# Optimization experiments

Hardware: AMD Instinct MI355X
Metric: run time of the kernel (lower is better)

The kernel has to match this reference:

```python
import jax, jax.numpy as jnp
import numpy as np

ROPE_BASE = 10000.0

def _rope_cos_sin(T, d, dtype):
    inv_freq = 1.0 / (ROPE_BASE ** (jnp.arange(0, d, 2, dtype=jnp.float32) / d))
    t = jnp.arange(T, dtype=jnp.float32)
    freqs = t[:, None] * inv_freq[None, :]           # [T, d/2]
    emb = jnp.concatenate([freqs, freqs], axis=-1)   # [T, d]
    return jnp.cos(emb).astype(dtype), jnp.sin(emb).astype(dtype)

def _rotate_half(x):
    x1, x2 = jnp.split(x, 2, axis=-1)
    return jnp.concatenate([-x2, x1], axis=-1)

def setup_inputs() -> dict:
    key = jax.random.key(0)
    k1, k2, k3, k4 = jax.random.split(key, 4)
    B, T, C, H = 4, 4096, 1024, 64
    x = jax.random.normal(k1, (B, T, C), dtype=jnp.float32)
    s = 1.0 / np.sqrt(C)
    Wq = jax.random.normal(k2, (H, C), dtype=jnp.float32) * s
    Wk = jax.random.normal(k3, (H, C), dtype=jnp.float32) * s
    Wv = jax.random.normal(k4, (H, C), dtype=jnp.float32) * s
    return {"x": x, "Wq": Wq, "Wk": Wk, "Wv": Wv}

def reference(x, Wq, Wk, Wv):
    B, T, C = x.shape
    H = Wq.shape[0]
    q = jnp.einsum('btc,hc->bth', x, Wq)
    k = jnp.einsum('btc,hc->bth', x, Wk)
    v = jnp.einsum('btc,hc->bth', x, Wv)
    cos, sin = _rope_cos_sin(T, H, x.dtype)
    q = q * cos + _rotate_half(q) * sin
    k = k * cos + _rotate_half(k) * sin
    # NOTE: original scales by dim_model**-0.5 (C), not head_size
    wei = jnp.einsum('bth,bsh->bts', q, k) * (C ** -0.5)
    causal = jnp.tril(jnp.ones((T, T), dtype=bool))
    wei = jnp.where(causal, wei, -jnp.inf)
    wei = jax.nn.softmax(wei, axis=-1)
    # dropout p=0.0 (identity)
    out = jnp.einsum('bts,bsh->bth', wei, v)
    return out
```

## Files before the change

kernel.cpp:

```cpp
#include <hip/hip_runtime.h>
#include <hip/hip_bf16.h>
#include <math.h>

typedef __attribute__((ext_vector_type(8))) __bf16 bf16x8;
typedef __attribute__((ext_vector_type(4))) float f32x4;
typedef __attribute__((ext_vector_type(16))) float f32x16;
typedef __attribute__((ext_vector_type(4))) float float4_t;
typedef __attribute__((ext_vector_type(4))) unsigned int uint4_t;

#define NB 4
#define TSEQ 4096
#define CD 1024
#define HD 64
#define NCH 8
#define CHT 8
#define QBL 16

static __device__ __forceinline__ unsigned short f2bf(float f) {
    union { float f; unsigned u; } v; v.f = f;
    unsigned r = v.u + 0x7fffu + ((v.u >> 16) & 1u);
    return (unsigned short)(r >> 16);
}
static __device__ __forceinline__ float bf2f(unsigned short u) {
    union { unsigned int i; float f; } v; v.i = ((unsigned int)u) << 16;
    return v.f;
}
static __device__ __forceinline__ unsigned int pk2(float a, float b) {
    union { __bf16 h[2]; unsigned int u; } x;
    x.h[0] = (__bf16)a; x.h[1] = (__bf16)b;
    return x.u;
}

__global__ __launch_bounds__(256) void wcvt_kernel(const float* __restrict__ wq,
                                                   const float* __restrict__ wk,
                                                   const float* __restrict__ wv,
                                                   unsigned short* __restrict__ wb) {
    int i = blockIdx.x * 256 + threadIdx.x;
    int j = i >> 10;
    int col = i & 1023;
    int jb = j >> 4, off = j & 15;
    int sub = ((jb & 1) << 5) | ((jb & 2) << 3);
    int srcrow = (jb < 8) ? (sub + off) : ((jb - 8) * 16 + off);
    const float* src = (jb < 4) ? wq : ((jb < 8) ? wk : wv);
    wb[i] = f2bf(src[srcrow * 1024 + col]);
}

__global__ __launch_bounds__(256) void qkv_kernel(const float* __restrict__ x,
                                                  const unsigned short* __restrict__ wb,
                                                  unsigned short* __restrict__ qo,
                                                  unsigned short* __restrict__ ko,
                                                  unsigned short* __restrict__ vt) {
    __shared__ unsigned short xs[64][72];
    __shared__ unsigned short ws[64][72];
    const int tid = threadIdx.x;
    const int wave = tid >> 6, lane = tid & 63;
    const int lr = lane & 15;
    const int lk = (lane >> 4) << 3;
    const int rowg = (lane >> 4) << 2;
    const int row0 = blockIdx.x * 64;
    const int cbi = blockIdx.y;
    const int cb = cbi * 64;

    f32x4 acc[4];
#pragma unroll
    for (int i = 0; i < 4; ++i) acc[i] = (f32x4){0.f, 0.f, 0.f, 0.f};

    const int sr = tid >> 2;
    const int sc = (tid & 3) << 4;

    for (int k0 = 0; k0 < CD; k0 += 64) {
        __syncthreads();
        {
            const float4_t* s4 =
                reinterpret_cast<const float4_t*>(x + (size_t)(row0 + sr) * CD + k0 + sc);
            float4_t f0 = s4[0], f1 = s4[1], f2 = s4[2], f3 = s4[3];
            uint4_t w0, w1;
            w0[0] = pk2(f0[0], f0[1]); w0[1] = pk2(f0[2], f0[3]);
            w0[2] = pk2(f1[0], f1[1]); w0[3] = pk2(f1[2], f1[3]);
            w1[0] = pk2(f2[0], f2[1]); w1[1] = pk2(f2[2], f2[3]);
            w1[2] = pk2(f3[0], f3[1]); w1[3] = pk2(f3[2], f3[3]);
            *reinterpret_cast<uint4_t*>(&xs[sr][sc]) = w0;
            *reinterpret_cast<uint4_t*>(&xs[sr][sc + 8]) = w1;
        }
        {
            const uint4_t* wsrc =
                reinterpret_cast<const uint4_t*>(wb + (size_t)(cb + sr) * CD + k0 + sc);
            *reinterpret_cast<uint4_t*>(&ws[sr][sc]) = wsrc[0];
            *reinterpret_cast<uint4_t*>(&ws[sr][sc + 8]) = wsrc[1];
        }
        __syncthreads();
#pragma unroll
        for (int kk = 0; kk < 2; ++kk) {
            bf16x8 a = *reinterpret_cast<const bf16x8*>(&xs[wave * 16 + lr][kk * 32 + lk]);
#pragma unroll
            for (int c = 0; c < 4; ++c) {
                bf16x8 bfr = *reinterpret_cast<const bf16x8*>(&ws[c * 16 + lr][kk * 32 + lk]);
                acc[c] = __builtin_amdgcn_mfma_f32_16x16x32_bf16(a, bfr, acc[c], 0, 0, 0);
            }
        }
    }

    const int gr0 = row0 + wave * 16 + rowg;
    const int bidx = gr0 >> 12;
    const int tb = gr0 & (TSEQ - 1);
    if (cbi < 2) {
        unsigned short* o = (cbi == 0) ? qo : ko;
        const float sc2 = (cbi == 0) ? 0.045084218764560315f : 1.0f;
        const float l2b = 0.4152410118609215f;
        const float invf0 = exp2f(-(float)lr * l2b);
        const float invf1 = exp2f(-(float)(lr + 16) * l2b);
#pragma unroll
        for (int r = 0; r < 4; ++r) {
            float t = (float)(tb + r);
            float s0, c0, s1, c1;
            sincosf(t * invf0, &s0, &c0);
            sincosf(t * invf1, &s1, &c1);
            size_t ro = (size_t)(gr0 + r) * HD;
            float lo, hi;
            lo = acc[0][r]; hi = acc[1][r];
            o[ro + 0 + lr]  = f2bf((lo * c0 - hi * s0) * sc2);
            o[ro + 32 + lr] = f2bf((hi * c0 + lo * s0) * sc2);
            lo = acc[2][r]; hi = acc[3][r];
            o[ro + 16 + lr] = f2bf((lo * c1 - hi * s1) * sc2);
            o[ro + 48 + lr] = f2bf((hi * c1 + lo * s1) * sc2);
        }
    } else {
#pragma unroll
        for (int r = 0; r < 4; ++r) {
            size_t vbase = (size_t)bidx * HD * TSEQ + (size_t)(tb + r);
            vt[vbase + (size_t)(0 + lr) * TSEQ]  = f2bf(acc[0][r]);
            vt[vbase + (size_t)(16 + lr) * TSEQ] = f2bf(acc[1][r]);
            vt[vbase + (size_t)(32 + lr) * TSEQ] = f2bf(acc[2][r]);
            vt[vbase + (size_t)(48 + lr) * TSEQ] = f2bf(acc[3][r]);
        }
    }
}

__global__ __launch_bounds__(512, 4) void attn_partial(const unsigned short* __restrict__ q,
                                                       const unsigned short* __restrict__ k,
                                                       const unsigned short* __restrict__ vt,
                                                       unsigned short* __restrict__ po,
                                                       float* __restrict__ pm,
                                                       float* __restrict__ pl) {
    const int chunk = blockIdx.x, qb = blockIdx.y, b = blockIdx.z;
    const int ktend_blk = 4 * qb + 3;
    const int kt0 = chunk * CHT;
    if (kt0 > ktend_blk) return;
    const int ktend = min(ktend_blk, kt0 + CHT - 1);

    __shared__ unsigned short ks[64][72];
    __shared__ unsigned short vs[64][72];
    const int tid = threadIdx.x;
    const int wave = tid >> 6, lane = tid & 63;
    const int l31 = lane & 31;
    const int h = lane >> 5;
    const int h8 = h << 3;
    const int qrow0 = qb * 256 + wave * 32;
    const int qpos = qrow0 + l31;

    const unsigned short* qb_ = q + ((size_t)(b * TSEQ + qpos)) * HD + h8;
    bf16x8 qf[4];
#pragma unroll
    for (int s = 0; s < 4; ++s)
        qf[s] = *reinterpret_cast<const bf16x8*>(qb_ + 16 * s);

    f32x16 oacc[2];
#pragma unroll
    for (int dt = 0; dt < 2; ++dt)
#pragma unroll
        for (int r = 0; r < 16; ++r) oacc[dt][r] = 0.f;
    float mreg = -1.0e30f;
    float lsum = 0.f;

    const int srow = tid >> 3;
    const int scol = (tid & 7) << 3;
    const unsigned short* kbase = k + (size_t)b * TSEQ * HD;
    const unsigned short* vbase = vt + (size_t)b * HD * TSEQ;
    uint4_t kr, vr;

    auto loadtile = [&](int kt) {
        const int s0l = kt * 64;
        kr = *reinterpret_cast<const uint4_t*>(kbase + (size_t)(s0l + srow) * HD + scol);
        vr = *reinterpret_cast<const uint4_t*>(vbase + (size_t)srow * TSEQ + s0l + scol);
    };

    loadtile(kt0);

    for (int kt = kt0; kt <= ktend; ++kt) {
        const int s0 = kt * 64;
        __syncthreads();
        *reinterpret_cast<uint4_t*>(&ks[srow][scol]) = kr;
        *reinterpret_cast<uint4_t*>(&vs[srow][scol]) = vr;
        __syncthreads();
        if (kt < ktend) loadtile(kt + 1);

        if (s0 > qrow0 + 31) continue;

        f32x16 sacc[2];
#pragma unroll
        for (int blk = 0; blk < 2; ++blk)
#pragma unroll
            for (int r = 0; r < 16; ++r) sacc[blk][r] = 0.f;
        __builtin_amdgcn_s_setprio(1);
#pragma unroll
        for (int s = 0; s < 4; ++s) {
            bf16x8 ka = *reinterpret_cast<const bf16x8*>(&ks[l31][16 * s + h8]);
            bf16x8 kb2 = *reinterpret_cast<const bf16x8*>(&ks[32 + l31][16 * s + h8]);
            sacc[0] = __builtin_amdgcn_mfma_f32_32x32x16_bf16(ka, qf[s], sacc[0], 0, 0, 0);
            sacc[1] = __builtin_amdgcn_mfma_f32_32x32x16_bf16(kb2, qf[s], sacc[1], 0, 0, 0);
        }
        __builtin_amdgcn_s_setprio(0);

        if (s0 + 63 > qrow0) {
#pragma unroll
            for (int blk = 0; blk < 2; ++blk)
#pragma unroll
                for (int r = 0; r < 16; ++r) {
                    int kvpos = s0 + 32 * blk + (r & 3) + ((r >> 2) << 3) + (h << 2);
                    if (kvpos > qpos) sacc[blk][r] = -INFINITY;
                }
        }

        float tm[8];
#pragma unroll
        for (int r = 0; r < 8; ++r)
            tm[r] = fmaxf(fmaxf(sacc[0][r], sacc[0][r + 8]),
                          fmaxf(sacc[1][r], sacc[1][r + 8]));
#pragma unroll
        for (int r = 0; r < 4; ++r) tm[r] = fmaxf(tm[r], tm[r + 4]);
        float mx = fmaxf(fmaxf(tm[0], tm[1]), fmaxf(tm[2], tm[3]));
        mx = fmaxf(mx, __shfl_xor(mx, 32, 64));

        const bool newmax = !__all(mx <= mreg + 7.0f);
        if (newmax) {
            float mnew = fmaxf(mreg, mx);
            float corr = __builtin_amdgcn_exp2f(mreg - mnew);
            mreg = mnew;
            lsum *= corr;
#pragma unroll
            for (int dt = 0; dt < 2; ++dt)
#pragma unroll
                for (int r = 0; r < 16; ++r) oacc[dt][r] *= corr;
        }

        float pvv[2][16];
#pragma unroll
        for (int blk = 0; blk < 2; ++blk)
#pragma unroll
            for (int r = 0; r < 16; ++r)
                pvv[blk][r] = __builtin_amdgcn_exp2f(sacc[blk][r] - mreg);
        float ts[8];
#pragma unroll
        for (int r = 0; r < 8; ++r)
            ts[r] = (pvv[0][r] + pvv[0][r + 8]) + (pvv[1][r] + pvv[1][r + 8]);
#pragma unroll
        for (int r = 0; r < 4; ++r) ts[r] += ts[r + 4];
        float psum = (ts[0] + ts[1]) + (ts[2] + ts[3]);
        psum += __shfl_xor(psum, 32, 64);
        lsum += psum;

        unsigned int cw[2][4][2];
#pragma unroll
        for (int blk = 0; blk < 2; ++blk)
#pragma unroll
            for (int G = 0; G < 4; ++G) {
                cw[blk][G][0] = pk2(pvv[blk][4 * G], pvv[blk][4 * G + 1]);
                cw[blk][G][1] = pk2(pvv[blk][4 * G + 2], pvv[blk][4 * G + 3]);
            }

        const bool hif = (h == 1);
        __builtin_amdgcn_s_setprio(1);
#pragma unroll
        for (int s = 0; s < 4; ++s) {
            const int blk = s >> 1, base = (s & 1) << 1;
            unsigned int a0 = cw[blk][base][0],     a1 = cw[blk][base][1];
            unsigned int b0 = cw[blk][base + 1][0], b1 = cw[blk][base + 1][1];
            unsigned int s0w = hif ? a0 : b0;
            unsigned int s1w = hif ? a1 : b1;
            unsigned int r0 = __shfl_xor(s0w, 32, 64);
            unsigned int r1 = __shfl_xor(s1w, 32, 64);
            uint4_t pw;
            pw[0] = hif ? r0 : a0;
            pw[1] = hif ? r1 : a1;
            pw[2] = hif ? b0 : r0;
            pw[3] = hif ? b1 : r1;
            bf16x8 pfrag = *reinterpret_cast<const bf16x8*>(&pw);
            bf16x8 v0 = *reinterpret_cast<const bf16x8*>(&vs[l31][16 * s + h8]);
            bf16x8 v1 = *reinterpret_cast<const bf16x8*>(&vs[32 + l31][16 * s + h8]);
            oacc[0] = __builtin_amdgcn_mfma_f32_32x32x16_bf16(v0, pfrag, oacc[0], 0, 0, 0);
            oacc[1] = __builtin_amdgcn_mfma_f32_32x32x16_bf16(v1, pfrag, oacc[1], 0, 0, 0);
        }
        __builtin_amdgcn_s_setprio(0);
    }

    const int slot = (((b << 4) + qb) << 3) + chunk;
    unsigned short* pob = po + (size_t)slot * 16384;
#pragma unroll
    for (int dt = 0; dt < 2; ++dt)
#pragma unroll
        for (int r = 0; r < 16; ++r) {
            int d = 32 * dt + (r & 3) + ((r >> 2) << 3) + (h << 2);
            pob[d * 256 + wave * 32 + l31] = f2bf(oacc[dt][r]);
        }
    if (h == 0) {
        pm[slot * 256 + wave * 32 + l31] = mreg;
        pl[slot * 256 + wave * 32 + l31] = lsum;
    }
}

__global__ __launch_bounds__(256) void attn_combine(const unsigned short* __restrict__ po,
                                                    const float* __restrict__ pm,
                                                    const float* __restrict__ pl,
                                                    float* __restrict__ out) {
    __shared__ float sm[64][17];
    const int bq = blockIdx.x;
    const int dg = blockIdx.y;
    const int qt = bq & 63;
    const int b = bq >> 6;
    const int qb = qt >> 2, quarter = qt & 3;
    const int nch = (4 * qb + 11) >> 3;
    const int qi = threadIdx.x & 63;
    const int jj = threadIdx.x >> 6;
    const int slotb = (((b << 4) + qb) << 3);
    const int qoff = quarter * 64 + qi;

    float pmv[NCH];
#pragma unroll
    for (int c = 0; c < NCH; ++c)
        pmv[c] = (c < nch) ? pm[(size_t)(slotb + c) * 256 + qoff] : -1.0e30f;
    float tmv[NCH];
#pragma unroll
    for (int c = 0; c < NCH; ++c) tmv[c] = pmv[c];
#pragma unroll
    for (int s = NCH / 2; s >= 1; s >>= 1)
#pragma unroll
        for (int c = 0; c < NCH / 2; ++c)
            if (c < s) tmv[c] = fmaxf(tmv[c], tmv[c + s]);
    const float M = tmv[0];

    float L = 0.f;
    float a0 = 0.f, a1 = 0.f, a2 = 0.f, a3 = 0.f;
    const int dbase = dg * 16 + jj * 4;
#pragma unroll 4
    for (int c = 0; c < nch; ++c) {
        float w = exp2f(pmv[c] - M);
        L += w * pl[(size_t)(slotb + c) * 256 + qoff];
        const unsigned short* p = po + (size_t)(slotb + c) * 16384 + dbase * 256 + qoff;
        a0 += w * bf2f(p[0]);
        a1 += w * bf2f(p[256]);
        a2 += w * bf2f(p[512]);
        a3 += w * bf2f(p[768]);
    }
    const float inv = 1.f / L;
    sm[qi][jj * 4 + 0] = a0 * inv;
    sm[qi][jj * 4 + 1] = a1 * inv;
    sm[qi][jj * 4 + 2] = a2 * inv;
    sm[qi][jj * 4 + 3] = a3 * inv;
    __syncthreads();
    const int row = threadIdx.x >> 2;
    const int c4 = (threadIdx.x & 3) << 2;
    float4_t f;
#pragma unroll
    for (int e = 0; e < 4; ++e) f[e] = sm[row][c4 + e];
    *reinterpret_cast<float4_t*>(out + (size_t)bq * 4096 + row * 64 + dg * 16 + c4) = f;
}

extern "C" void kernel_launch(void* const* d_in, const int* in_sizes, int n_in,
                              void* d_out, int out_size, void* d_ws, size_t ws_size,
                              hipStream_t stream) {
    const float* x = (const float*)d_in[0];
    const float* wq = (const float*)d_in[1];
    const float* wk = (const float*)d_in[2];
    const float* wv = (const float*)d_in[3];
    float* out = (float*)d_out;

    unsigned short* wb = (unsigned short*)d_ws;
    unsigned short* qb = wb + 3 * HD * CD;
    unsigned short* kb = qb + (size_t)NB * TSEQ * HD;
    unsigned short* vtb = kb + (size_t)NB * TSEQ * HD;
    unsigned short* pob = vtb + (size_t)NB * TSEQ * HD;
    float* pm = (float*)(pob + (size_t)512 * 16384);
    float* pl = pm + (size_t)512 * 256;

    wcvt_kernel<<<768, 256, 0, stream>>>(wq, wk, wv, wb);
    qkv_kernel<<<dim3(256, 3), 256, 0, stream>>>(x, wb, qb, kb, vtb);
    attn_partial<<<dim3(NCH, QBL, NB), 512, 0, stream>>>(qb, kb, vtb, pob, pm, pl);
    attn_combine<<<dim3(NB * 64, 4), 256, 0, stream>>>(pob, pm, pl, out);
}
```

Before: 61.26 us.

## Prefetch projection tiles into registers and double-buffer K/V in attention

The projection GEMM now loads the next x and W tiles into registers while MFMAs run on the current LDS tile, hiding global load latency. The attention partial kernel now uses two LDS buffers for K and V. It writes the next tile into the alternate buffer and issues the global load two tiles ahead, which removes one barrier per iteration. This doubles the attention kernel's LDS footprint and raises register pressure, which may lower occupancy.

```diff
diff --git a/kernel.cpp b/kernel.cpp
--- a/kernel.cpp
+++ b/kernel.cpp
@@ -68,27 +68,34 @@
     const int sr = tid >> 2;
     const int sc = (tid & 3) << 4;
 
+    float4_t xf0, xf1, xf2, xf3;
+    uint4_t wf0, wf1;
+    auto loadregs = [&](int k0) {
+        const float4_t* s4 =
+            reinterpret_cast<const float4_t*>(x + (size_t)(row0 + sr) * CD + k0 + sc);
+        xf0 = s4[0]; xf1 = s4[1]; xf2 = s4[2]; xf3 = s4[3];
+        const uint4_t* wsrc =
+            reinterpret_cast<const uint4_t*>(wb + (size_t)(cb + sr) * CD + k0 + sc);
+        wf0 = wsrc[0]; wf1 = wsrc[1];
+    };
+
+    loadregs(0);
+
     for (int k0 = 0; k0 < CD; k0 += 64) {
         __syncthreads();
         {
-            const float4_t* s4 =
-                reinterpret_cast<const float4_t*>(x + (size_t)(row0 + sr) * CD + k0 + sc);
-            float4_t f0 = s4[0], f1 = s4[1], f2 = s4[2], f3 = s4[3];
             uint4_t w0, w1;
-            w0[0] = pk2(f0[0], f0[1]); w0[1] = pk2(f0[2], f0[3]);
-            w0[2] = pk2(f1[0], f1[1]); w0[3] = pk2(f1[2], f1[3]);
-            w1[0] = pk2(f2[0], f2[1]); w1[1] = pk2(f2[2], f2[3]);
-            w1[2] = pk2(f3[0], f3[1]); w1[3] = pk2(f3[2], f3[3]);
+            w0[0] = pk2(xf0[0], xf0[1]); w0[1] = pk2(xf0[2], xf0[3]);
+            w0[2] = pk2(xf1[0], xf1[1]); w0[3] = pk2(xf1[2], xf1[3]);
+            w1[0] = pk2(xf2[0], xf2[1]); w1[1] = pk2(xf2[2], xf2[3]);
+            w1[2] = pk2(xf3[0], xf3[1]); w1[3] = pk2(xf3[2], xf3[3]);
             *reinterpret_cast<uint4_t*>(&xs[sr][sc]) = w0;
             *reinterpret_cast<uint4_t*>(&xs[sr][sc + 8]) = w1;
-        }
-        {
-            const uint4_t* wsrc =
-                reinterpret_cast<const uint4_t*>(wb + (size_t)(cb + sr) * CD + k0 + sc);
-            *reinterpret_cast<uint4_t*>(&ws[sr][sc]) = wsrc[0];
-            *reinterpret_cast<uint4_t*>(&ws[sr][sc + 8]) = wsrc[1];
+            *reinterpret_cast<uint4_t*>(&ws[sr][sc]) = wf0;
+            *reinterpret_cast<uint4_t*>(&ws[sr][sc + 8]) = wf1;
         }
         __syncthreads();
+        if (k0 + 64 < CD) loadregs(k0 + 64);
 #pragma unroll
         for (int kk = 0; kk < 2; ++kk) {
             bf16x8 a = *reinterpret_cast<const bf16x8*>(&xs[wave * 16 + lr][kk * 32 + lk]);
@@ -147,9 +154,10 @@
     const int kt0 = chunk * CHT;
     if (kt0 > ktend_blk) return;
     const int ktend = min(ktend_blk, kt0 + CHT - 1);
-
-    __shared__ unsigned short ks[64][72];
-    __shared__ unsigned short vs[64][72];
+    const int nt = ktend - kt0 + 1;
+
+    __shared__ unsigned short ks[2][64][72];
+    __shared__ unsigned short vs[2][64][72];
     const int tid = threadIdx.x;
     const int wave = tid >> 6, lane = tid & 63;
     const int l31 = lane & 31;
@@ -183,114 +191,123 @@
         kr = *reinterpret_cast<const uint4_t*>(kbase + (size_t)(s0l + srow) * HD + scol);
         vr = *reinterpret_cast<const uint4_t*>(vbase + (size_t)srow * TSEQ + s0l + scol);
     };
+    auto writetile = [&](int p) {
+        *reinterpret_cast<uint4_t*>(&ks[p][srow][scol]) = kr;
+        *reinterpret_cast<uint4_t*>(&vs[p][srow][scol]) = vr;
+    };
 
     loadtile(kt0);
-
-    for (int kt = kt0; kt <= ktend; ++kt) {
+    writetile(0);
+    if (nt > 1) loadtile(kt0 + 1);
+    __syncthreads();
+
+    for (int it = 0; it < nt; ++it) {
+        const int kt = kt0 + it;
         const int s0 = kt * 64;
+        const int p = it & 1;
+        if (it + 1 < nt) {
+            writetile(p ^ 1);
+            if (it + 2 < nt) loadtile(kt + 2);
+        }
+
+        if (s0 <= qrow0 + 31) {
+            f32x16 sacc[2];
+#pragma unroll
+            for (int blk = 0; blk < 2; ++blk)
+#pragma unroll
+                for (int r = 0; r < 16; ++r) sacc[blk][r] = 0.f;
+            __builtin_amdgcn_s_setprio(1);
+#pragma unroll
+            for (int s = 0; s < 4; ++s) {
+                bf16x8 ka = *reinterpret_cast<const bf16x8*>(&ks[p][l31][16 * s + h8]);
+                bf16x8 kb2 = *reinterpret_cast<const bf16x8*>(&ks[p][32 + l31][16 * s + h8]);
+                sacc[0] = __builtin_amdgcn_mfma_f32_32x32x16_bf16(ka, qf[s], sacc[0], 0, 0, 0);
+                sacc[1] = __builtin_amdgcn_mfma_f32_32x32x16_bf16(kb2, qf[s], sacc[1], 0, 0, 0);
+            }
+            __builtin_amdgcn_s_setprio(0);
+
+            if (s0 + 63 > qrow0) {
+#pragma unroll
+                for (int blk = 0; blk < 2; ++blk)
+#pragma unroll
+                    for (int r = 0; r < 16; ++r) {
+                        int kvpos = s0 + 32 * blk + (r & 3) + ((r >> 2) << 3) + (h << 2);
+                        if (kvpos > qpos) sacc[blk][r] = -INFINITY;
+                    }
+            }
+
+            float tm[8];
+#pragma unroll
+            for (int r = 0; r < 8; ++r)
+                tm[r] = fmaxf(fmaxf(sacc[0][r], sacc[0][r + 8]),
+                              fmaxf(sacc[1][r], sacc[1][r + 8]));
+#pragma unroll
+            for (int r = 0; r < 4; ++r) tm[r] = fmaxf(tm[r], tm[r + 4]);
+            float mx = fmaxf(fmaxf(tm[0], tm[1]), fmaxf(tm[2], tm[3]));
+            mx = fmaxf(mx, __shfl_xor(mx, 32, 64));
+
+            const bool newmax = !__all(mx <= mreg + 7.0f);
+            if (newmax) {
+                float mnew = fmaxf(mreg, mx);
+                float corr = __builtin_amdgcn_exp2f(mreg - mnew);
+                mreg = mnew;
+                lsum *= corr;
+#pragma unroll
+                for (int dt = 0; dt < 2; ++dt)
+#pragma unroll
+                    for (int r = 0; r < 16; ++r) oacc[dt][r] *= corr;
+            }
+
+            float pvv[2][16];
+#pragma unroll
+            for (int blk = 0; blk < 2; ++blk)
+#pragma unroll
+                for (int r = 0; r < 16; ++r)
+                    pvv[blk][r] = __builtin_amdgcn_exp2f(sacc[blk][r] - mreg);
+            float ts[8];
+#pragma unroll
+            for (int r = 0; r < 8; ++r)
+                ts[r] = (pvv[0][r] + pvv[0][r + 8]) + (pvv[1][r] + pvv[1][r + 8]);
+#pragma unroll
+            for (int r = 0; r < 4; ++r) ts[r] += ts[r + 4];
+            float psum = (ts[0] + ts[1]) + (ts[2] + ts[3]);
+            psum += __shfl_xor(psum, 32, 64);
+            lsum += psum;
+
+            unsigned int cw[2][4][2];
+#pragma unroll
+            for (int blk = 0; blk < 2; ++blk)
+#pragma unroll
+                for (int G = 0; G < 4; ++G) {
+                    cw[blk][G][0] = pk2(pvv[blk][4 * G], pvv[blk][4 * G + 1]);
+                    cw[blk][G][1] = pk2(pvv[blk][4 * G + 2], pvv[blk][4 * G + 3]);
+                }
+
+            const bool hif = (h == 1);
+            __builtin_amdgcn_s_setprio(1);
+#pragma unroll
+            for (int s = 0; s < 4; ++s) {
+                const int blk = s >> 1, base = (s & 1) << 1;
+                unsigned int a0 = cw[blk][base][0],     a1 = cw[blk][base][1];
+                unsigned int b0 = cw[blk][base + 1][0], b1 = cw[blk][base + 1][1];
+                unsigned int s0w = hif ? a0 : b0;
+                unsigned int s1w = hif ? a1 : b1;
+                unsigned int r0 = __shfl_xor(s0w, 32, 64);
+                unsigned int r1 = __shfl_xor(s1w, 32, 64);
+                uint4_t pw;
+                pw[0] = hif ? r0 : a0;
+                pw[1] = hif ? r1 : a1;
+                pw[2] = hif ? b0 : r0;
+                pw[3] = hif ? b1 : r1;
+                bf16x8 pfrag = *reinterpret_cast<const bf16x8*>(&pw);
+                bf16x8 v0 = *reinterpret_cast<const bf16x8*>(&vs[p][l31][16 * s + h8]);
+                bf16x8 v1 = *reinterpret_cast<const bf16x8*>(&vs[p][32 + l31][16 * s + h8]);
+                oacc[0] = __builtin_amdgcn_mfma_f32_32x32x16_bf16(v0, pfrag, oacc[0], 0, 0, 0);
+                oacc[1] = __builtin_amdgcn_mfma_f32_32x32x16_bf16(v1, pfrag, oacc[1], 0, 0, 0);
+            }
+            __builtin_amdgcn_s_setprio(0);
+        }
         __syncthreads();
-        *reinterpret_cast<uint4_t*>(&ks[srow][scol]) = kr;
-        *reinterpret_cast<uint4_t*>(&vs[srow][scol]) = vr;
-        __syncthreads();
-        if (kt < ktend) loadtile(kt + 1);
-
-        if (s0 > qrow0 + 31) continue;
-
-        f32x16 sacc[2];
-#pragma unroll
-        for (int blk = 0; blk < 2; ++blk)
-#pragma unroll
-            for (int r = 0; r < 16; ++r) sacc[blk][r] = 0.f;
-        __builtin_amdgcn_s_setprio(1);
-#pragma unroll
-        for (int s = 0; s < 4; ++s) {
-            bf16x8 ka = *reinterpret_cast<const bf16x8*>(&ks[l31][16 * s + h8]);
-            bf16x8 kb2 = *reinterpret_cast<const bf16x8*>(&ks[32 + l31][16 * s + h8]);
-            sacc[0] = __builtin_amdgcn_mfma_f32_32x32x16_bf16(ka, qf[s], sacc[0], 0, 0, 0);
-            sacc[1] = __builtin_amdgcn_mfma_f32_32x32x16_bf16(kb2, qf[s], sacc[1], 0, 0, 0);
-        }
-        __builtin_amdgcn_s_setprio(0);
-
-        if (s0 + 63 > qrow0) {
-#pragma unroll
-            for (int blk = 0; blk < 2; ++blk)
-#pragma unroll
-                for (int r = 0; r < 16; ++r) {
-                    int kvpos = s0 + 32 * blk + (r & 3) + ((r >> 2) << 3) + (h << 2);
-                    if (kvpos > qpos) sacc[blk][r] = -INFINITY;
-                }
-        }
-
-        float tm[8];
-#pragma unroll
-        for (int r = 0; r < 8; ++r)
-            tm[r] = fmaxf(fmaxf(sacc[0][r], sacc[0][r + 8]),
-                          fmaxf(sacc[1][r], sacc[1][r + 8]));
-#pragma unroll
-        for (int r = 0; r < 4; ++r) tm[r] = fmaxf(tm[r], tm[r + 4]);
-        float mx = fmaxf(fmaxf(tm[0], tm[1]), fmaxf(tm[2], tm[3]));
-        mx = fmaxf(mx, __shfl_xor(mx, 32, 64));
-
-        const bool newmax = !__all(mx <= mreg + 7.0f);
-        if (newmax) {
-            float mnew = fmaxf(mreg, mx);
-            float corr = __builtin_amdgcn_exp2f(mreg - mnew);
-            mreg = mnew;
-            lsum *= corr;
-#pragma unroll
-            for (int dt = 0; dt < 2; ++dt)
-#pragma unroll
-                for (int r = 0; r < 16; ++r) oacc[dt][r] *= corr;
-        }
-
-        float pvv[2][16];
-#pragma unroll
-        for (int blk = 0; blk < 2; ++blk)
-#pragma unroll
-            for (int r = 0; r < 16; ++r)
-                pvv[blk][r] = __builtin_amdgcn_exp2f(sacc[blk][r] - mreg);
-        float ts[8];
-#pragma unroll
-        for (int r = 0; r < 8; ++r)
-            ts[r] = (pvv[0][r] + pvv[0][r + 8]) + (pvv[1][r] + pvv[1][r + 8]);
-#pragma unroll
-        for (int r = 0; r < 4; ++r) ts[r] += ts[r + 4];
-        float psum = (ts[0] + ts[1]) + (ts[2] + ts[3]);
-        psum += __shfl_xor(psum, 32, 64);
-        lsum += psum;
-
-        unsigned int cw[2][4][2];
-#pragma unroll
-        for (int blk = 0; blk < 2; ++blk)
-#pragma unroll
-            for (int G = 0; G < 4; ++G) {
-                cw[blk][G][0] = pk2(pvv[blk][4 * G], pvv[blk][4 * G + 1]);
-                cw[blk][G][1] = pk2(pvv[blk][4 * G + 2], pvv[blk][4 * G + 3]);
-            }
-
-        const bool hif = (h == 1);
-        __builtin_amdgcn_s_setprio(1);
-#pragma unroll
-        for (int s = 0; s < 4; ++s) {
-            const int blk = s >> 1, base = (s & 1) << 1;
-            unsigned int a0 = cw[blk][base][0],     a1 = cw[blk][base][1];
-            unsigned int b0 = cw[blk][base + 1][0], b1 = cw[blk][base + 1][1];
-            unsigned int s0w = hif ? a0 : b0;
-            unsigned int s1w = hif ? a1 : b1;
-            unsigned int r0 = __shfl_xor(s0w, 32, 64);
-            unsigned int r1 = __shfl_xor(s1w, 32, 64);
-            uint4_t pw;
-            pw[0] = hif ? r0 : a0;
-            pw[1] = hif ? r1 : a1;
-            pw[2] = hif ? b0 : r0;
-            pw[3] = hif ? b1 : r1;
-            bf16x8 pfrag = *reinterpret_cast<const bf16x8*>(&pw);
-            bf16x8 v0 = *reinterpret_cast<const bf16x8*>(&vs[l31][16 * s + h8]);
-            bf16x8 v1 = *reinterpret_cast<const bf16x8*>(&vs[32 + l31][16 * s + h8]);
-            oacc[0] = __builtin_amdgcn_mfma_f32_32x32x16_bf16(v0, pfrag, oacc[0], 0, 0, 0);
-            oacc[1] = __builtin_amdgcn_mfma_f32_32x32x16_bf16(v1, pfrag, oacc[1], 0, 0, 0);
-        }
-        __builtin_amdgcn_s_setprio(0);
     }
 
     const int slot = (((b << 4) + qb) << 3) + chunk;
```

Result: no change. 61.37 us (+0.2%).
